# Kernel optimization log

Measured on AMD Instinct MI355X. Metric: run time of the kernel, lower is better.

## Reference

```python
import jax, jax.numpy as jnp
import numpy as np

ALPHA = 0.5        # damping from conf['alpha']
MAX_ITERS = 30     # fixed-point iterations (conf uses up to 150 with eps early-exit)
GN_GROUPS = 3
GN_EPS = 1e-5
SLOPE = 0.01       # F.leaky_relu default negative_slope


def _conv(x, w, b, pad):
    y = jax.lax.conv_general_dilated(
        x, w, window_strides=(1, 1), padding=[(pad, pad), (pad, pad)],
        dimension_numbers=("NCHW", "OIHW", "NCHW"))
    return y + b[None, :, None, None]


def _leaky(x):
    return jnp.where(x >= 0, x, SLOPE * x)


def _groupnorm(x, gamma, beta):
    N, C, H, W = x.shape
    xg = x.reshape(N, GN_GROUPS, C // GN_GROUPS, H, W)
    mu = xg.mean(axis=(2, 3, 4), keepdims=True)
    var = xg.var(axis=(2, 3, 4), keepdims=True)
    xg = (xg - mu) * jax.lax.rsqrt(var + GN_EPS)
    x = xg.reshape(N, C, H, W)
    return x * gamma[None, :, None, None] + beta[None, :, None, None]


def setup_inputs() -> dict:
    key = jax.random.key(0)
    ks = jax.random.split(key, 8)
    image = jax.random.normal(ks[0], (1024, 3, 32, 32), dtype=jnp.float32)
    # Unit params (small init keeps the fixed-point iteration contractive)
    w1 = jax.random.normal(ks[1], (6, 8, 5, 5), dtype=jnp.float32) * 0.05
    b1 = jnp.zeros((6,), jnp.float32)
    gamma = jnp.ones((6,), jnp.float32)
    beta = jnp.zeros((6,), jnp.float32)
    w2 = jax.random.normal(ks[2], (5, 6, 5, 5), dtype=jnp.float32) * 0.05
    b2 = jnp.zeros((5,), jnp.float32)
    # detection head: Conv2d(5, 10, 32, padding=0) -> full-image conv
    wh = jax.random.normal(ks[3], (10, 5, 32, 32), dtype=jnp.float32) * 0.01
    bh = jnp.zeros((10,), jnp.float32)
    return {"image": image, "w1": w1, "b1": b1, "gamma": gamma, "beta": beta,
            "w2": w2, "b2": b2, "wh": wh, "bh": bh}


def reference(image, w1, b1, gamma, beta, w2, b2, wh, bh):
    N = image.shape[0]
    z0 = jnp.zeros((N, 5, 32, 32), image.dtype)

    def unit(z):
        zx = jnp.concatenate([z, image], axis=1)
        h = _groupnorm(_leaky(_conv(zx, w1, b1, 2)), gamma, beta)
        return _leaky(_conv(h, w2, b2, 2))

    def step(z, _):
        z = (1.0 - ALPHA) * z + ALPHA * unit(z)
        return z, None

    z, _ = jax.lax.scan(step, z0, None, length=MAX_ITERS)
    return _conv(z, wh, bh, 0)
```

## Files before the change

### kernel.cpp

```cpp
#include <hip/hip_runtime.h>
#include <hip/hip_fp16.h>


typedef _Float16 half8 __attribute__((ext_vector_type(8)));
typedef float f32x4 __attribute__((ext_vector_type(4)));

__device__ __forceinline__ unsigned pk2(float a, float b) {
    __half2 h = __float22half2_rn(make_float2(a, b));
    return *reinterpret_cast<unsigned*>(&h);
}
__device__ __forceinline__ float2 up2(unsigned u) {
    __half2 h = *reinterpret_cast<__half2*>(&u);
    return __half22float2(h);
}
__device__ __forceinline__ unsigned hmul2(unsigned a, unsigned b) {
    __half2 r = __hmul2(*reinterpret_cast<__half2*>(&a), *reinterpret_cast<__half2*>(&b));
    return *reinterpret_cast<unsigned*>(&r);
}
__device__ __forceinline__ float lrelu(float x) { return fmaxf(x, 0.01f * x); }
__device__ __forceinline__ int bofs(int y, int x) {
    return ((y * 36 + x) * 16) ^ ((x & 8) << 1);
}

__global__ void pack_weights(const float* __restrict__ w1,
                             const float* __restrict__ w2,
                             unsigned* __restrict__ ws)
{
    int t = blockIdx.x * 256 + threadIdx.x;
    if (t < 512) {
        int c = t >> 6, l = t & 63;
        int row = l & 15, tgw = l >> 4;
        int dx = row >> 3, oc = row & 7, tap = 4 * c + tgw;
        unsigned q[4];
        #pragma unroll
        for (int d = 0; d < 4; ++d) {
            float v0 = 0.f, v1 = 0.f;
            if (oc < 6 && tap < 30) {
                int ty = tap / 6, kx = tap % 6 - dx;
                if (kx >= 0 && kx < 5) {
                    v0 = w1[(oc * 8 + 2 * d) * 25 + ty * 5 + kx];
                    v1 = w1[(oc * 8 + 2 * d + 1) * 25 + ty * 5 + kx];
                }
            }
            q[d] = pk2(v0, v1);
        }
        *(uint4*)&ws[t * 4] = make_uint4(q[0], q[1], q[2], q[3]);
    } else if (t < 1024) {
        int u = t - 512;
        int c = u >> 6, l = u & 63;
        int row = l & 15, tgw = l >> 4;
        int dx = row >> 3, oc = row & 7, tap = 4 * c + tgw;
        unsigned q[4];
        #pragma unroll
        for (int d = 0; d < 4; ++d) {
            float v0 = 0.f, v1 = 0.f;
            if (oc < 5 && tap < 30) {
                int ty = tap / 6, kx = tap % 6 - dx;
                if (kx >= 0 && kx < 5) {
                    if (2 * d < 6)     v0 = w2[(oc * 6 + 2 * d) * 25 + ty * 5 + kx];
                    if (2 * d + 1 < 6) v1 = w2[(oc * 6 + 2 * d + 1) * 25 + ty * 5 + kx];
                }
            }
            q[d] = pk2(v0, v1);
        }
        *(uint4*)&ws[2048 + u * 4] = make_uint4(q[0], q[1], q[2], q[3]);
    } else if (t < 1054) {
        int idx = t - 1024;
        int oc = idx / 6, ch = idx % 6;
        float s = 0.f;
        for (int tap = 0; tap < 25; ++tap) s += w2[(oc * 6 + ch) * 25 + tap];
        ((float*)ws)[4096 + idx] = s;
    }
}

__global__ __launch_bounds__(256, 2)
void deq_kernel(const float* __restrict__ image,
                const unsigned* __restrict__ wks,
                const float* __restrict__ b1,
                const float* __restrict__ gam, const float* __restrict__ bet,
                const float* __restrict__ b2,
                const float* __restrict__ wh, const float* __restrict__ bh,
                float* __restrict__ out)
{
    __shared__ __align__(16) unsigned zxb[36 * 36 * 4];
    __shared__ __align__(16) unsigned hbb[36 * 36 * 4];
    __shared__ __align__(16) unsigned wl2[2048];
    __shared__ float red[48];
    __shared__ float s2s[32];

    const int n    = blockIdx.x;
    const int tid  = threadIdx.x;
    const int lane = tid & 63;
    const int wid  = tid >> 6;
    const int col  = lane & 15;
    const int tg   = lane >> 4;
    const int dxl  = tg >> 1;
    const int sub  = tg & 1;

    for (int p = tid; p < 36 * 36 * 4; p += 256) { zxb[p] = 0u; hbb[p] = 0u; }
    for (int p = tid; p < 2048; p += 256) wl2[p] = wks[2048 + p];
    if (tid < 30) s2s[tid] = ((const float*)wks)[4096 + tid];
    __syncthreads();

    {
        const int yy = tid >> 3, xx0 = (tid & 7) << 2;
        float4 i0 = *(const float4*)&image[(n * 3 + 0) * 1024 + yy * 32 + xx0];
        float4 i1 = *(const float4*)&image[(n * 3 + 1) * 1024 + yy * 32 + xx0];
        float4 i2 = *(const float4*)&image[(n * 3 + 2) * 1024 + yy * 32 + xx0];
        float a0[4] = {i0.x, i0.y, i0.z, i0.w};
        float a1[4] = {i1.x, i1.y, i1.z, i1.w};
        float a2[4] = {i2.x, i2.y, i2.z, i2.w};
        #pragma unroll
        for (int i = 0; i < 4; ++i) {
            unsigned* bp = (unsigned*)((char*)zxb + bofs(yy + 2, xx0 + 2 + i));
            bp[2] = pk2(0.f, a0[i]);
            bp[3] = pk2(a1[i], a2[i]);
        }
    }

    uint4 cw1[8];
    #pragma unroll
    for (int c = 0; c < 8; ++c)
        cw1[c] = *(const uint4*)&wks[(c * 64 + lane) * 4];

    int toff[8];
    #pragma unroll
    for (int c = 0; c < 8; ++c) {
        int t = 4 * c + tg;
        int ty = 0, tx = 0;
        if (t < 30) { ty = t / 6; tx = t % 6; }
        int xr = 2 * col + tx;
        toff[c] = ty * 576 + ((xr * 16) ^ ((xr & 8) << 1));
    }

    float b1q[4], b2q[4];
    #pragma unroll
    for (int r = 0; r < 4; ++r) {
        int oc = (tg * 4 + r) & 7;
        b1q[r] = (oc < 6) ? b1[oc] : 0.f;
        b2q[r] = (oc < 5) ? b2[oc] : 0.f;
    }
    const f32x4 ai1 = {b1q[0], b1q[1], b1q[2], b1q[3]};

    __syncthreads();

    const char* zb = (const char*)zxb;
    const char* hb = (const char*)hbb;
    const int ay0 = wid << 3;
    const int wlo = lane << 2;

    #pragma unroll 1
    for (int it = 0; it < 30; ++it) {
        float ps_lo = 0.f, ps_hi = 0.f, pq_lo = 0.f, pq_hi = 0.f;
        #pragma unroll
        for (int half = 0; half < 2; ++half) {
            const int ayh = ay0 + half * 4;
            f32x4 acc[4];
            #pragma unroll
            for (int g = 0; g < 4; ++g) acc[g] = ai1;
            #pragma unroll
            for (int c = 0; c < 8; ++c) {
                half8 wf = __builtin_bit_cast(half8, cw1[c]);
                #pragma unroll
                for (int g = 0; g < 4; ++g) {
                    half8 pv = *(const half8*)(zb + (ayh + g) * 576 + toff[c]);
                    acc[g] = __builtin_amdgcn_mfma_f32_16x16x32_f16(wf, pv, acc[g], 0, 0, 0);
                }
            }
            #pragma unroll
            for (int g = 0; g < 4; ++g) {
                float h0 = lrelu(acc[g][0]), h1 = lrelu(acc[g][1]);
                float h2 = lrelu(acc[g][2]), h3 = lrelu(acc[g][3]);
                ps_lo += h0 + h1;  pq_lo = fmaf(h0, h0, fmaf(h1, h1, pq_lo));
                ps_hi += h2 + h3;  pq_hi = fmaf(h2, h2, fmaf(h3, h3, pq_hi));
                char* wp = (char*)hbb + bofs(ayh + g + 2, 2 * col + dxl + 2) + sub * 8;
                *(uint2*)wp = make_uint2(pk2(h0, h1), pk2(h2, h3));
            }
        }

        #pragma unroll
        for (int m = 1; m <= 8; m <<= 1) {
            ps_lo += __shfl_xor(ps_lo, m); ps_hi += __shfl_xor(ps_hi, m);
            pq_lo += __shfl_xor(pq_lo, m); pq_hi += __shfl_xor(pq_hi, m);
        }
        ps_lo += __shfl_xor(ps_lo, 32); ps_hi += __shfl_xor(ps_hi, 32);
        pq_lo += __shfl_xor(pq_lo, 32); pq_hi += __shfl_xor(pq_hi, 32);
        if (lane == 0)  { red[wid * 8 + 0] = ps_lo; red[wid * 8 + 1] = ps_hi;
                          red[wid * 8 + 4] = pq_lo; red[wid * 8 + 5] = pq_hi; }
        if (lane == 16) { red[wid * 8 + 2] = ps_lo; red[wid * 8 + 6] = pq_lo; }
        __syncthreads();

        float scv[6], shv[6];
        #pragma unroll
        for (int g3 = 0; g3 < 3; ++g3) {
            float s = 0.f, q = 0.f;
            #pragma unroll
            for (int w = 0; w < 4; ++w) { s += red[w * 8 + g3]; q += red[w * 8 + 4 + g3]; }
            float mean = s * (1.f / 2048.f);
            float var  = q * (1.f / 2048.f) - mean * mean;
            float inv  = rsqrtf(var + 1e-5f);
            #pragma unroll
            for (int k = 0; k < 2; ++k) {
                int c = 2 * g3 + k;
                scv[c] = inv * gam[c];
                shv[c] = bet[c] - mean * scv[c];
            }
        }
        f32x4 ai2;
        #pragma unroll
        for (int r = 0; r < 4; ++r) {
            int ocr = (tg * 4 + r) & 7;
            int base = (ocr < 5) ? ocr * 6 : 0;
            float db = 0.f;
            #pragma unroll
            for (int ch = 0; ch < 6; ++ch) db = fmaf(s2s[base + ch], shv[ch], db);
            ai2[r] = b2q[r] + ((ocr < 5) ? db : 0.f);
        }
        unsigned sp0 = pk2(scv[0], scv[1]), sp1 = pk2(scv[2], scv[3]), sp2 = pk2(scv[4], scv[5]);
        {
            float ph[6];
            #pragma unroll
            for (int c = 0; c < 6; ++c) {
                float rs = (fabsf(scv[c]) > 1e-20f) ? 1.f / scv[c] : 0.f;
                ph[c] = -shv[c] * rs;
            }
            uint4 padq = make_uint4(pk2(ph[0], ph[1]), pk2(ph[2], ph[3]), pk2(ph[4], ph[5]), 0u);
            for (int t = tid; t < 272; t += 256) {
                int row, cc;
                if (t < 72)       { row = t / 36;             cc = t % 36; }
                else if (t < 144) { row = 34 + (t - 72) / 36; cc = (t - 72) % 36; }
                else {
                    int q4 = t - 144;
                    row = 2 + (q4 >> 2);
                    int c4 = q4 & 3;
                    cc = (c4 < 2) ? c4 : c4 + 32;
                }
                *(uint4*)((char*)hbb + bofs(row, cc)) = padq;
            }
        }
        __syncthreads();

        #pragma unroll
        for (int half = 0; half < 2; ++half) {
            const int ayh = ay0 + half * 4;
            f32x4 acc[4];
            #pragma unroll
            for (int g = 0; g < 4; ++g) acc[g] = ai2;
            #pragma unroll
            for (int c = 0; c < 8; ++c) {
                uint4 wr = *(const uint4*)&wl2[c * 256 + wlo];
                uint4 wsc;
                wsc.x = hmul2(wr.x, sp0);
                wsc.y = hmul2(wr.y, sp1);
                wsc.z = hmul2(wr.z, sp2);
                wsc.w = 0u;
                half8 wf = __builtin_bit_cast(half8, wsc);
                #pragma unroll
                for (int g = 0; g < 4; ++g) {
                    half8 pv = *(const half8*)(hb + (ayh + g) * 576 + toff[c]);
                    acc[g] = __builtin_amdgcn_mfma_f32_16x16x32_f16(wf, pv, acc[g], 0, 0, 0);
                }
            }
            #pragma unroll
            for (int g = 0; g < 4; ++g) {
                char* zp = (char*)zxb + bofs(ayh + g + 2, 2 * col + dxl + 2);
                if (sub == 0) {
                    uint2 zo = *(uint2*)zp;
                    float2 za = up2(zo.x), zc = up2(zo.y);
                    float z0 = 0.5f * za.x + 0.5f * lrelu(acc[g][0]);
                    float z1 = 0.5f * za.y + 0.5f * lrelu(acc[g][1]);
                    float z2 = 0.5f * zc.x + 0.5f * lrelu(acc[g][2]);
                    float z3 = 0.5f * zc.y + 0.5f * lrelu(acc[g][3]);
                    *(uint2*)zp = make_uint2(pk2(z0, z1), pk2(z2, z3));
                } else {
                    _Float16* pz = (_Float16*)(zp + 8);
                    float z4 = 0.5f * (float)pz[0] + 0.5f * lrelu(acc[g][0]);
                    pz[0] = (_Float16)z4;
                }
            }
        }
        __syncthreads();
    }

    {
        const int yy = tid >> 3, xx0 = (tid & 7) << 2;
        float zf[5][4];
        #pragma unroll
        for (int i = 0; i < 4; ++i) {
            const unsigned* bp = (const unsigned*)((const char*)zxb + bofs(yy + 2, xx0 + 2 + i));
            float2 f0 = up2(bp[0]), f1 = up2(bp[1]), f2 = up2(bp[2]);
            zf[0][i] = f0.x; zf[1][i] = f0.y; zf[2][i] = f1.x; zf[3][i] = f1.y; zf[4][i] = f2.x;
        }
        float ho[10];
        #pragma unroll
        for (int o = 0; o < 10; ++o) ho[o] = 0.f;
        #pragma unroll
        for (int c = 0; c < 5; ++c) {
            #pragma unroll
            for (int o = 0; o < 10; ++o) {
                float4 wv = *(const float4*)&wh[(o * 5 + c) * 1024 + yy * 32 + xx0];
                ho[o] = fmaf(zf[c][0], wv.x, ho[o]);
                ho[o] = fmaf(zf[c][1], wv.y, ho[o]);
                ho[o] = fmaf(zf[c][2], wv.z, ho[o]);
                ho[o] = fmaf(zf[c][3], wv.w, ho[o]);
            }
        }
        #pragma unroll
        for (int m = 1; m < 64; m <<= 1) {
            #pragma unroll
            for (int o = 0; o < 10; ++o) ho[o] += __shfl_xor(ho[o], m);
        }
        if (lane == 0) {
            #pragma unroll
            for (int o = 0; o < 10; ++o) red[wid * 10 + o] = ho[o];
        }
    }
    __syncthreads();
    if (tid < 10)
        out[n * 10 + tid] = red[tid] + red[10 + tid] + red[20 + tid] + red[30 + tid] + bh[tid];
}

extern "C" void kernel_launch(void* const* d_in, const int* in_sizes, int n_in,
                              void* d_out, int out_size, void* d_ws, size_t ws_size,
                              hipStream_t stream) {
    const float* image = (const float*)d_in[0];
    const float* w1    = (const float*)d_in[1];
    const float* b1    = (const float*)d_in[2];
    const float* gam   = (const float*)d_in[3];
    const float* bet   = (const float*)d_in[4];
    const float* w2    = (const float*)d_in[5];
    const float* b2    = (const float*)d_in[6];
    const float* wh    = (const float*)d_in[7];
    const float* bh    = (const float*)d_in[8];
    float* out = (float*)d_out;
    unsigned* ws = (unsigned*)d_ws;

    pack_weights<<<5, 256, 0, stream>>>(w1, w2, ws);

    const int N = in_sizes[0] / (3 * 32 * 32);
    deq_kernel<<<N, 256, 0, stream>>>(image, ws, b1, gam, bet, b2, wh, bh, out);
}
```

Measured before the change: 376.7 us.

## Reuse each loaded input row across all kernel rows in MFMA convolution loops

Changes the implicit-GEMM tap decomposition from 8 chunks of 4 arbitrary taps to a 5x2 grid (kernel row × half of the x-taps). Each B fragment (a padded input row slice) is now loaded once and fed to up to 5 output-row accumulators, cutting LDS reads per MFMA. The cost is 10 MFMAs per output row group instead of 8 (more padding work), 8 live accumulators, and weights for both convs moved to LDS and reloaded each iteration.

After: 352.7 us. 1.07x faster.

```diff
diff --git a/kernel.cpp b/kernel.cpp
--- a/kernel.cpp
+++ b/kernel.cpp
@@ -4,6 +4,12 @@
 
 typedef _Float16 half8 __attribute__((ext_vector_type(8)));
 typedef float f32x4 __attribute__((ext_vector_type(4)));
+
+#define PLANE 5184
+#define HB    5184
+#define WL1   10368
+#define WL2   12928
+#define NLDS  15488
 
 __device__ __forceinline__ unsigned pk2(float a, float b) {
     __half2 h = __float22half2_rn(make_float2(a, b));
@@ -27,49 +33,45 @@
                              unsigned* __restrict__ ws)
 {
     int t = blockIdx.x * 256 + threadIdx.x;
-    if (t < 512) {
+    if (t < 640) {
         int c = t >> 6, l = t & 63;
-        int row = l & 15, tgw = l >> 4;
-        int dx = row >> 3, oc = row & 7, tap = 4 * c + tgw;
+        int row = l & 15, tg = l >> 4;
+        int dx = row >> 3, oc = row & 7;
+        int ty = c >> 1, tx = 4 * (c & 1) + tg, kx = tx - dx;
         unsigned q[4];
         #pragma unroll
         for (int d = 0; d < 4; ++d) {
             float v0 = 0.f, v1 = 0.f;
-            if (oc < 6 && tap < 30) {
-                int ty = tap / 6, kx = tap % 6 - dx;
-                if (kx >= 0 && kx < 5) {
-                    v0 = w1[(oc * 8 + 2 * d) * 25 + ty * 5 + kx];
-                    v1 = w1[(oc * 8 + 2 * d + 1) * 25 + ty * 5 + kx];
-                }
+            if (oc < 6 && kx >= 0 && kx < 5) {
+                v0 = w1[(oc * 8 + 2 * d) * 25 + ty * 5 + kx];
+                v1 = w1[(oc * 8 + 2 * d + 1) * 25 + ty * 5 + kx];
             }
             q[d] = pk2(v0, v1);
         }
         *(uint4*)&ws[t * 4] = make_uint4(q[0], q[1], q[2], q[3]);
-    } else if (t < 1024) {
-        int u = t - 512;
+    } else if (t < 1280) {
+        int u = t - 640;
         int c = u >> 6, l = u & 63;
-        int row = l & 15, tgw = l >> 4;
-        int dx = row >> 3, oc = row & 7, tap = 4 * c + tgw;
+        int row = l & 15, tg = l >> 4;
+        int dx = row >> 3, oc = row & 7;
+        int ty = c >> 1, tx = 4 * (c & 1) + tg, kx = tx - dx;
         unsigned q[4];
         #pragma unroll
         for (int d = 0; d < 4; ++d) {
             float v0 = 0.f, v1 = 0.f;
-            if (oc < 5 && tap < 30) {
-                int ty = tap / 6, kx = tap % 6 - dx;
-                if (kx >= 0 && kx < 5) {
-                    if (2 * d < 6)     v0 = w2[(oc * 6 + 2 * d) * 25 + ty * 5 + kx];
-                    if (2 * d + 1 < 6) v1 = w2[(oc * 6 + 2 * d + 1) * 25 + ty * 5 + kx];
-                }
+            if (oc < 5 && kx >= 0 && kx < 5) {
+                if (2 * d < 6)     v0 = w2[(oc * 6 + 2 * d) * 25 + ty * 5 + kx];
+                if (2 * d + 1 < 6) v1 = w2[(oc * 6 + 2 * d + 1) * 25 + ty * 5 + kx];
             }
             q[d] = pk2(v0, v1);
         }
-        *(uint4*)&ws[2048 + u * 4] = make_uint4(q[0], q[1], q[2], q[3]);
-    } else if (t < 1054) {
-        int idx = t - 1024;
+        *(uint4*)&ws[2560 + u * 4] = make_uint4(q[0], q[1], q[2], q[3]);
+    } else if (t < 1310) {
+        int idx = t - 1280;
         int oc = idx / 6, ch = idx % 6;
         float s = 0.f;
         for (int tap = 0; tap < 25; ++tap) s += w2[(oc * 6 + ch) * 25 + tap];
-        ((float*)ws)[4096 + idx] = s;
+        ((float*)ws)[5120 + idx] = s;
     }
 }
 
@@ -82,9 +84,7 @@
                 const float* __restrict__ wh, const float* __restrict__ bh,
                 float* __restrict__ out)
 {
-    __shared__ __align__(16) unsigned zxb[36 * 36 * 4];
-    __shared__ __align__(16) unsigned hbb[36 * 36 * 4];
-    __shared__ __align__(16) unsigned wl2[2048];
+    __shared__ __align__(16) unsigned lds[NLDS];
     __shared__ float red[48];
     __shared__ float s2s[32];
 
@@ -97,9 +97,12 @@
     const int dxl  = tg >> 1;
     const int sub  = tg & 1;
 
-    for (int p = tid; p < 36 * 36 * 4; p += 256) { zxb[p] = 0u; hbb[p] = 0u; }
-    for (int p = tid; p < 2048; p += 256) wl2[p] = wks[2048 + p];
-    if (tid < 30) s2s[tid] = ((const float*)wks)[4096 + tid];
+    for (int p = tid; p < 2 * PLANE; p += 256) lds[p] = 0u;
+    for (int p = tid; p < 2560; p += 256) {
+        lds[WL1 + p] = wks[p];
+        lds[WL2 + p] = wks[2560 + p];
+    }
+    if (tid < 30) s2s[tid] = ((const float*)wks)[5120 + tid];
     __syncthreads();
 
     {
@@ -112,25 +115,17 @@
         float a2[4] = {i2.x, i2.y, i2.z, i2.w};
         #pragma unroll
         for (int i = 0; i < 4; ++i) {
-            unsigned* bp = (unsigned*)((char*)zxb + bofs(yy + 2, xx0 + 2 + i));
+            unsigned* bp = (unsigned*)((char*)lds + bofs(yy + 2, xx0 + 2 + i));
             bp[2] = pk2(0.f, a0[i]);
             bp[3] = pk2(a1[i], a2[i]);
         }
     }
 
-    uint4 cw1[8];
+    int sx2[2];
     #pragma unroll
-    for (int c = 0; c < 8; ++c)
-        cw1[c] = *(const uint4*)&wks[(c * 64 + lane) * 4];
-
-    int toff[8];
-    #pragma unroll
-    for (int c = 0; c < 8; ++c) {
-        int t = 4 * c + tg;
-        int ty = 0, tx = 0;
-        if (t < 30) { ty = t / 6; tx = t % 6; }
-        int xr = 2 * col + tx;
-        toff[c] = ty * 576 + ((xr * 16) ^ ((xr & 8) << 1));
+    for (int txh = 0; txh < 2; ++txh) {
+        int x = 2 * col + 4 * txh + tg;
+        sx2[txh] = (x * 16) ^ ((x & 8) << 1);
     }
 
     float b1q[4], b2q[4];
@@ -144,38 +139,47 @@
 
     __syncthreads();
 
-    const char* zb = (const char*)zxb;
-    const char* hb = (const char*)hbb;
+    const char* zb  = (const char*)lds;
+    const char* hbB = (const char*)lds + HB * 4;
     const int ay0 = wid << 3;
     const int wlo = lane << 2;
 
     #pragma unroll 1
     for (int it = 0; it < 30; ++it) {
+        uint4 f1[10];
+        #pragma unroll
+        for (int c = 0; c < 10; ++c)
+            f1[c] = *(const uint4*)&lds[WL1 + c * 256 + wlo];
+
+        f32x4 acc[8];
+        #pragma unroll
+        for (int g = 0; g < 8; ++g) acc[g] = ai1;
+
+        #pragma unroll
+        for (int pr = 0; pr < 12; ++pr) {
+            const char* rowp = zb + (ay0 + pr) * 576;
+            #pragma unroll
+            for (int txh = 0; txh < 2; ++txh) {
+                half8 pv = *(const half8*)(rowp + sx2[txh]);
+                #pragma unroll
+                for (int ty = 0; ty < 5; ++ty) {
+                    const int g = pr - ty;
+                    if (g >= 0 && g < 8)
+                        acc[g] = __builtin_amdgcn_mfma_f32_16x16x32_f16(
+                            __builtin_bit_cast(half8, f1[ty * 2 + txh]), pv, acc[g], 0, 0, 0);
+                }
+            }
+        }
+
         float ps_lo = 0.f, ps_hi = 0.f, pq_lo = 0.f, pq_hi = 0.f;
         #pragma unroll
-        for (int half = 0; half < 2; ++half) {
-            const int ayh = ay0 + half * 4;
-            f32x4 acc[4];
-            #pragma unroll
-            for (int g = 0; g < 4; ++g) acc[g] = ai1;
-            #pragma unroll
-            for (int c = 0; c < 8; ++c) {
-                half8 wf = __builtin_bit_cast(half8, cw1[c]);
-                #pragma unroll
-                for (int g = 0; g < 4; ++g) {
-                    half8 pv = *(const half8*)(zb + (ayh + g) * 576 + toff[c]);
-                    acc[g] = __builtin_amdgcn_mfma_f32_16x16x32_f16(wf, pv, acc[g], 0, 0, 0);
-                }
-            }
-            #pragma unroll
-            for (int g = 0; g < 4; ++g) {
-                float h0 = lrelu(acc[g][0]), h1 = lrelu(acc[g][1]);
-                float h2 = lrelu(acc[g][2]), h3 = lrelu(acc[g][3]);
-                ps_lo += h0 + h1;  pq_lo = fmaf(h0, h0, fmaf(h1, h1, pq_lo));
-                ps_hi += h2 + h3;  pq_hi = fmaf(h2, h2, fmaf(h3, h3, pq_hi));
-                char* wp = (char*)hbb + bofs(ayh + g + 2, 2 * col + dxl + 2) + sub * 8;
-                *(uint2*)wp = make_uint2(pk2(h0, h1), pk2(h2, h3));
-            }
+        for (int g = 0; g < 8; ++g) {
+            float h0 = lrelu(acc[g][0]), h1 = lrelu(acc[g][1]);
+            float h2 = lrelu(acc[g][2]), h3 = lrelu(acc[g][3]);
+            ps_lo += h0 + h1;  pq_lo = fmaf(h0, h0, fmaf(h1, h1, pq_lo));
+            ps_hi += h2 + h3;  pq_hi = fmaf(h2, h2, fmaf(h3, h3, pq_hi));
+            char* wp = (char*)lds + HB * 4 + bofs(ay0 + g + 2, 2 * col + dxl + 2) + sub * 8;
+            *(uint2*)wp = make_uint2(pk2(h0, h1), pk2(h2, h3));
         }
 
         #pragma unroll
@@ -235,48 +239,54 @@
                     int c4 = q4 & 3;
                     cc = (c4 < 2) ? c4 : c4 + 32;
                 }
-                *(uint4*)((char*)hbb + bofs(row, cc)) = padq;
+                *(uint4*)((char*)lds + HB * 4 + bofs(row, cc)) = padq;
             }
         }
         __syncthreads();
 
-        #pragma unroll
-        for (int half = 0; half < 2; ++half) {
-            const int ayh = ay0 + half * 4;
-            f32x4 acc[4];
-            #pragma unroll
-            for (int g = 0; g < 4; ++g) acc[g] = ai2;
-            #pragma unroll
-            for (int c = 0; c < 8; ++c) {
-                uint4 wr = *(const uint4*)&wl2[c * 256 + wlo];
-                uint4 wsc;
-                wsc.x = hmul2(wr.x, sp0);
-                wsc.y = hmul2(wr.y, sp1);
-                wsc.z = hmul2(wr.z, sp2);
-                wsc.w = 0u;
-                half8 wf = __builtin_bit_cast(half8, wsc);
+        uint4 f2[10];
+        #pragma unroll
+        for (int c = 0; c < 10; ++c) {
+            uint4 wr = *(const uint4*)&lds[WL2 + c * 256 + wlo];
+            f2[c].x = hmul2(wr.x, sp0);
+            f2[c].y = hmul2(wr.y, sp1);
+            f2[c].z = hmul2(wr.z, sp2);
+            f2[c].w = 0u;
+        }
+        #pragma unroll
+        for (int g = 0; g < 8; ++g) acc[g] = ai2;
+
+        #pragma unroll
+        for (int pr = 0; pr < 12; ++pr) {
+            const char* rowp = hbB + (ay0 + pr) * 576;
+            #pragma unroll
+            for (int txh = 0; txh < 2; ++txh) {
+                half8 pv = *(const half8*)(rowp + sx2[txh]);
                 #pragma unroll
-                for (int g = 0; g < 4; ++g) {
-                    half8 pv = *(const half8*)(hb + (ayh + g) * 576 + toff[c]);
-                    acc[g] = __builtin_amdgcn_mfma_f32_16x16x32_f16(wf, pv, acc[g], 0, 0, 0);
+                for (int ty = 0; ty < 5; ++ty) {
+                    const int g = pr - ty;
+                    if (g >= 0 && g < 8)
+                        acc[g] = __builtin_amdgcn_mfma_f32_16x16x32_f16(
+                            __builtin_bit_cast(half8, f2[ty * 2 + txh]), pv, acc[g], 0, 0, 0);
                 }
             }
-            #pragma unroll
-            for (int g = 0; g < 4; ++g) {
-                char* zp = (char*)zxb + bofs(ayh + g + 2, 2 * col + dxl + 2);
-                if (sub == 0) {
-                    uint2 zo = *(uint2*)zp;
-                    float2 za = up2(zo.x), zc = up2(zo.y);
-                    float z0 = 0.5f * za.x + 0.5f * lrelu(acc[g][0]);
-                    float z1 = 0.5f * za.y + 0.5f * lrelu(acc[g][1]);
-                    float z2 = 0.5f * zc.x + 0.5f * lrelu(acc[g][2]);
-                    float z3 = 0.5f * zc.y + 0.5f * lrelu(acc[g][3]);
-                    *(uint2*)zp = make_uint2(pk2(z0, z1), pk2(z2, z3));
-                } else {
-                    _Float16* pz = (_Float16*)(zp + 8);
-                    float z4 = 0.5f * (float)pz[0] + 0.5f * lrelu(acc[g][0]);
-                    pz[0] = (_Float16)z4;
-                }
+        }
+
+        #pragma unroll
+        for (int g = 0; g < 8; ++g) {
+            char* zp = (char*)lds + bofs(ay0 + g + 2, 2 * col + dxl + 2);
+            if (sub == 0) {
+                uint2 zo = *(uint2*)zp;
+                float2 za = up2(zo.x), zc = up2(zo.y);
+                float z0 = 0.5f * za.x + 0.5f * lrelu(acc[g][0]);
+                float z1 = 0.5f * za.y + 0.5f * lrelu(acc[g][1]);
+                float z2 = 0.5f * zc.x + 0.5f * lrelu(acc[g][2]);
+                float z3 = 0.5f * zc.y + 0.5f * lrelu(acc[g][3]);
+                *(uint2*)zp = make_uint2(pk2(z0, z1), pk2(z2, z3));
+            } else {
+                _Float16* pz = (_Float16*)(zp + 8);
+                float z4 = 0.5f * (float)pz[0] + 0.5f * lrelu(acc[g][0]);
+                pz[0] = (_Float16)z4;
             }
         }
         __syncthreads();
@@ -287,7 +297,7 @@
         float zf[5][4];
         #pragma unroll
         for (int i = 0; i < 4; ++i) {
-            const unsigned* bp = (const unsigned*)((const char*)zxb + bofs(yy + 2, xx0 + 2 + i));
+            const unsigned* bp = (const unsigned*)((const char*)lds + bofs(yy + 2, xx0 + 2 + i));
             float2 f0 = up2(bp[0]), f1 = up2(bp[1]), f2 = up2(bp[2]);
             zf[0][i] = f0.x; zf[1][i] = f0.y; zf[2][i] = f1.x; zf[3][i] = f1.y; zf[4][i] = f2.x;
         }
@@ -335,7 +345,7 @@
     float* out = (float*)d_out;
     unsigned* ws = (unsigned*)d_ws;
 
-    pack_weights<<<5, 256, 0, stream>>>(w1, w2, ws);
+    pack_weights<<<6, 256, 0, stream>>>(w1, w2, ws);
 
     const int N = in_sizes[0] / (3 * 32 * 32);
     deq_kernel<<<N, 256, 0, stream>>>(image, ws, b1, gam, bet, b2, wh, bh, out);
```
